# Performance work log

Hardware: AMD Instinct MI355X
Metric: run time of the kernel (lower is better)

The kernel has to match this reference:

```python
import jax, jax.numpy as jnp
import numpy as np

B, S, D, E, K = 4, 4096, 1024, 8, 2
H = 2 * D  # expert hidden dim


def setup_inputs() -> dict:
    key = jax.random.key(0)
    ks = jax.random.split(key, 7)
    scale = 0.02
    return {
        "x": jax.random.normal(ks[0], (B, S, D), dtype=jnp.float32),
        "router_w": jax.random.normal(ks[1], (D, E), dtype=jnp.float32) * scale,
        "router_b": jnp.zeros((E,), dtype=jnp.float32),
        "w1": jax.random.normal(ks[2], (E, D, H), dtype=jnp.float32) * scale,
        "b1": jnp.zeros((E, H), dtype=jnp.float32),
        "w2": jax.random.normal(ks[3], (E, H, D), dtype=jnp.float32) * scale,
        "b2": jnp.zeros((E, D), dtype=jnp.float32),
    }


def reference(x, router_w, router_b, w1, b1, w2, b2):
    # Router: softmax over experts, then top-k and renormalize
    logits = jnp.einsum("bsd,de->bse", x, router_w) + router_b
    probs = jax.nn.softmax(logits, axis=-1)
    top_p, top_i = jax.lax.top_k(probs, K)             # [B,S,K]
    top_p = top_p / jnp.sum(top_p, axis=-1, keepdims=True)

    out = jnp.zeros_like(x)
    for e in range(E):
        # gate weight for expert e per token (0 if not routed)
        gate = jnp.sum(top_p * (top_i == e), axis=-1)  # [B,S]
        h = jax.nn.relu(jnp.einsum("bsd,dh->bsh", x, w1[e]) + b1[e])
        y = jnp.einsum("bsh,hd->bsd", h, w2[e]) + b2[e]
        out = out + y * gate[..., None]
    return out
```

## Files before the change

kernel.cpp:

```cpp
#include <hip/hip_runtime.h>
#include <cstdio>
#include <cstdint>

#define N_TOK 16384
#define DIM   1024
#define NEXP  8
#define HID   2048
#define BK    32

typedef __attribute__((ext_vector_type(8))) short bf16x8;
typedef __attribute__((ext_vector_type(4))) float f32x4;

__device__ inline ushort f2bf(float f) {
  uint32_t u = __float_as_uint(f);
  uint32_t r = (u + 0x7fffu + ((u >> 16) & 1u)) >> 16;
  return (ushort)r;
}
__device__ inline float bf2f(ushort u) { return __uint_as_float(((uint32_t)u) << 16); }

__device__ __forceinline__ void gload_lds16(const void* g, void* l) {
  __builtin_amdgcn_global_load_lds((const __attribute__((address_space(1))) void*)g,
                                   (__attribute__((address_space(3))) void*)l, 16, 0, 0);
}

#define WAITV(N) asm volatile("s_waitcnt vmcnt(" #N ")" ::: "memory")
#define PBAR()  do { __builtin_amdgcn_s_barrier(); __builtin_amdgcn_sched_barrier(0); } while (0)

__global__ __launch_bounds__(256) void router_kernel(
    const float* __restrict__ x, const float* __restrict__ rw,
    const float* __restrict__ rb, int* __restrict__ blkcnt,
    int* __restrict__ tok_e, float* __restrict__ tok_g,
    ushort* __restrict__ xb) {
  __shared__ float wT[NEXP][DIM];
  __shared__ int hist[NEXP];
  if (threadIdx.x < NEXP) hist[threadIdx.x] = 0;
  for (int i = threadIdx.x; i < NEXP * DIM; i += 256) {
    int d = i >> 3, e = i & 7;
    wT[e][d] = rw[i];
  }
  __syncthreads();
  int wave = threadIdx.x >> 6, lane = threadIdx.x & 63;
  int t0 = blockIdx.x * 16 + wave * 4;
#pragma unroll
  for (int it = 0; it < 4; ++it) {
    int t = t0 + it;
    const float* xr = x + (size_t)t * DIM;
    float acc[NEXP];
#pragma unroll
    for (int e = 0; e < NEXP; ++e) acc[e] = 0.f;
#pragma unroll
    for (int j = 0; j < DIM / 64; ++j) {
      int d = lane + j * 64;
      float xv = xr[d];
#pragma unroll
      for (int e = 0; e < NEXP; ++e) acc[e] += xv * wT[e][d];
    }
    float lg[NEXP];
#pragma unroll
    for (int e = 0; e < NEXP; ++e) {
      float v = acc[e];
      for (int o = 32; o > 0; o >>= 1) v += __shfl_xor(v, o);
      lg[e] = v + rb[e];
    }
    int i0 = 0; float m0 = lg[0];
#pragma unroll
    for (int e = 1; e < NEXP; ++e) if (lg[e] > m0) { m0 = lg[e]; i0 = e; }
    int i1 = -1; float m1 = -3.4e38f;
#pragma unroll
    for (int e = 0; e < NEXP; ++e) if (e != i0 && lg[e] > m1) { m1 = lg[e]; i1 = e; }
    float g0 = 1.f / (1.f + expf(m1 - m0));
    float g1 = 1.f - g0;
    if (lane == 0) {
      tok_e[2 * t] = i0; tok_e[2 * t + 1] = i1;
      tok_g[2 * t] = g0; tok_g[2 * t + 1] = g1;
      atomicAdd(&hist[i0], 1); atomicAdd(&hist[i1], 1);
    }
  }
  {
    const float* xs = x + (size_t)blockIdx.x * 16 * DIM;
    ushort* xd = xb + (size_t)blockIdx.x * 16 * DIM;
    for (int i = threadIdx.x; i < 16 * DIM / 4; i += 256) {
      float4 v = *(const float4*)(xs + i * 4);
      ushort4 u = { f2bf(v.x), f2bf(v.y), f2bf(v.z), f2bf(v.w) };
      *(ushort4*)(xd + i * 4) = u;
    }
  }
  __syncthreads();
  if (threadIdx.x < NEXP) blkcnt[blockIdx.x * NEXP + threadIdx.x] = hist[threadIdx.x];
}

__global__ __launch_bounds__(512) void scan_kernel(const int* __restrict__ blkcnt,
                                                   int* __restrict__ blkbase,
                                                   int* __restrict__ offs) {
  __shared__ int s[64][8];
  __shared__ int chunkoff[64][8];
  __shared__ int offsh[8];
  int tid = threadIdx.x;
  int e = tid & 7, chunk = tid >> 3;
  int b0 = chunk * 16;
  int csum = 0;
#pragma unroll
  for (int b = 0; b < 16; ++b) csum += blkcnt[(b0 + b) * 8 + e];
  s[chunk][e] = csum;
  __syncthreads();
  int wave = tid >> 6, lane = tid & 63;
  int v = s[lane][wave];
  for (int o = 1; o < 64; o <<= 1) {
    int u = __shfl_up(v, o);
    if (lane >= o) v += u;
  }
  if (lane == 63) offsh[wave] = v;
  chunkoff[lane][wave] = v - s[lane][wave];
  __syncthreads();
  if (tid < 9) {
    int oe = 0;
    for (int j = 0; j < tid && j < 8; ++j) oe += offsh[j];
    offs[tid] = oe;
  }
  int oe2 = 0;
#pragma unroll
  for (int j = 0; j < 8; ++j) oe2 += (j < e) ? offsh[j] : 0;
  int base = oe2 + chunkoff[chunk][e];
  for (int b = 0; b < 16; ++b) {
    int idx = (b0 + b) * 8 + e;
    int c = blkcnt[idx];
    blkbase[idx] = base;
    base += c;
  }
}

__global__ __launch_bounds__(64) void gather_kernel(
    const int* __restrict__ tok_e, const float* __restrict__ tok_g,
    const int* __restrict__ blkbase, int* __restrict__ slot_token,
    float* __restrict__ slot_gate) {
  __shared__ int lcnt[NEXP];
  int tid = threadIdx.x, blk = blockIdx.x;
  if (tid < NEXP) lcnt[tid] = blkbase[blk * NEXP + tid];
  __syncthreads();
  if (tid < 32) {
    int t = blk * 16 + (tid >> 1);
    int k = tid & 1;
    int e = tok_e[2 * t + k];
    int s = atomicAdd(&lcnt[e], 1);
    slot_token[s] = t | (k << 16);
    slot_gate[s] = tok_g[2 * t + k];
  }
}

template <int R, int C>
__global__ __launch_bounds__(256) void transpose_cvt(const float* __restrict__ src,
                                                     ushort* __restrict__ dst) {
  __shared__ float tile[64][65];
  int e = blockIdx.z;
  const float* s = src + (size_t)e * R * C;
  ushort* d = dst + (size_t)e * R * C;
  int r0 = blockIdx.y * 64, c0 = blockIdx.x * 64;
  int tid = threadIdx.x;
#pragma unroll
  for (int i = 0; i < 4; ++i) {
    int idx = i * 256 + tid;
    int r = idx >> 4, c4 = (idx & 15) * 4;
    float4 v = *(const float4*)(s + (size_t)(r0 + r) * C + c0 + c4);
    tile[r][c4] = v.x; tile[r][c4 + 1] = v.y; tile[r][c4 + 2] = v.z; tile[r][c4 + 3] = v.w;
  }
  __syncthreads();
#pragma unroll
  for (int i = 0; i < 2; ++i) {
    int idx = i * 256 + tid;
    int orow = idx >> 3, g = (idx & 7) * 8;
    uint32_t p0 = (uint32_t)f2bf(tile[g + 0][orow]) | ((uint32_t)f2bf(tile[g + 1][orow]) << 16);
    uint32_t p1 = (uint32_t)f2bf(tile[g + 2][orow]) | ((uint32_t)f2bf(tile[g + 3][orow]) << 16);
    uint32_t p2 = (uint32_t)f2bf(tile[g + 4][orow]) | ((uint32_t)f2bf(tile[g + 5][orow]) << 16);
    uint32_t p3 = (uint32_t)f2bf(tile[g + 6][orow]) | ((uint32_t)f2bf(tile[g + 7][orow]) << 16);
    int4 v = { (int)p0, (int)p1, (int)p2, (int)p3 };
    *(int4*)(d + (size_t)(c0 + orow) * R + r0 + g) = v;
  }
}


__global__ __launch_bounds__(512, 1) void gemm1_kernel(
    const ushort* __restrict__ xb, const ushort* __restrict__ w1T,
    const float* __restrict__ b1, const int* __restrict__ offs,
    const int* __restrict__ slot_token, ushort* __restrict__ h) {
  int flat = blockIdx.x;
  int swz = (flat & 7) * 512 + (flat >> 3);
  int e = swz >> 9;
  int rem = swz & 511;
  int mt = rem >> 3;
  int nt = rem & 7;
  int off = offs[e];
  int cn = offs[e + 1] - off;
  if (mt * 256 >= cn) return;

  __shared__ __align__(16) ushort AB[4 * 16384];
  __shared__ int toks[256];
  int tid = threadIdx.x;
  if (tid < 256) {
    int r = mt * 256 + tid;
    toks[tid] = slot_token[off + (r < cn ? r : 0)] & 0xffff;
  }
  __syncthreads();
  int wave = tid >> 6, lane = tid & 63;
  int wm = (wave >> 2) * 128, wn = (wave & 3) * 64;

  const ushort* Bsrc = w1T + (size_t)e * HID * DIM + (size_t)(nt * 256) * DIM;
  int colsw = ((lane & 3) ^ ((lane >> 3) & 3)) * 8;
  int r0 = wave * 16 + (lane >> 2);
  const ushort* ag0 = xb + (size_t)toks[r0] * DIM + colsw;
  const ushort* ag1 = xb + (size_t)toks[128 + r0] * DIM + colsw;
  const ushort* bg0 = Bsrc + (size_t)r0 * DIM + colsw;
  const ushort* bg1 = Bsrc + (size_t)(128 + r0) * DIM + colsw;
  int ldsA0 = (wave * 16) * BK;
  int ldsA1 = (128 + wave * 16) * BK;
  int ldsB0 = 8192 + ldsA0;
  int ldsB1 = 8192 + ldsA1;

  f32x4 acc[8][4];
#pragma unroll
  for (int i = 0; i < 8; ++i)
#pragma unroll
    for (int j = 0; j < 4; ++j) acc[i][j] = (f32x4){0.f, 0.f, 0.f, 0.f};

  int rdo = (lane & 15) * 64 + ((((lane >> 4) & 3) << 4) ^ ((((lane & 15) >> 1) & 3) << 4));

  auto stage = [&](int buf) {
    ushort* lb = &AB[buf * 16384];
    gload_lds16(ag0, lb + ldsA0); ag0 += BK;
    gload_lds16(ag1, lb + ldsA1); ag1 += BK;
    gload_lds16(bg0, lb + ldsB0); bg0 += BK;
    gload_lds16(bg1, lb + ldsB1); bg1 += BK;
  };
  auto compute = [&](int buf) {
    const char* base = (const char*)AB + (size_t)buf * 32768;
    bf16x8 a[8], b[4];
#pragma unroll
    for (int mi = 0; mi < 8; ++mi)
      a[mi] = *(const bf16x8*)(base + (wm + mi * 16) * 64 + rdo);
#pragma unroll
    for (int ni = 0; ni < 4; ++ni)
      b[ni] = *(const bf16x8*)(base + 16384 + (wn + ni * 16) * 64 + rdo);
    __builtin_amdgcn_s_setprio(1);
#pragma unroll
    for (int mi = 0; mi < 8; ++mi)
#pragma unroll
      for (int ni = 0; ni < 4; ++ni)
        acc[mi][ni] = __builtin_amdgcn_mfma_f32_16x16x32_bf16(a[mi], b[ni], acc[mi][ni], 0, 0, 0);
    __builtin_amdgcn_s_setprio(0);
  };

  const int T = DIM / BK;
  stage(0); stage(1); stage(2);
  for (int t4 = 0; t4 < T - 4; t4 += 4) {
    WAITV(8); PBAR(); stage(3); compute(0);
    WAITV(8); PBAR(); stage(0); compute(1);
    WAITV(8); PBAR(); stage(1); compute(2);
    WAITV(8); PBAR(); stage(2); compute(3);
  }
  WAITV(8); PBAR(); stage(3); compute(0);
  WAITV(8); PBAR(); compute(1);
  WAITV(4); PBAR(); compute(2);
  WAITV(0); PBAR(); compute(3);

  __syncthreads();
  char* Cb = (char*)AB;
  int ln = lane & 15, lg4 = (lane >> 4) * 4;
#pragma unroll
  for (int ni = 0; ni < 4; ++ni) {
    int coll = wn + ni * 16 + ln;
    float bias = b1[(size_t)e * HID + nt * 256 + coll];
#pragma unroll
    for (int mi = 0; mi < 8; ++mi) {
#pragma unroll
      for (int rg = 0; rg < 4; ++rg) {
        int row = wm + mi * 16 + lg4 + rg;
        float v = fmaxf(acc[mi][ni][rg] + bias, 0.f);
        int slot = (coll >> 3) ^ (row & 7);
        *(ushort*)(Cb + row * 512 + slot * 16 + (coll & 7) * 2) = f2bf(v);
      }
    }
  }
  __syncthreads();
#pragma unroll
  for (int rr = 0; rr < 16; ++rr) {
    int row = rr * 16 + (tid >> 5);
    int scol = tid & 31;
    int4 v = *(const int4*)(Cb + row * 512 + ((scol ^ (row & 7)) << 4));
    int r = mt * 256 + row;
    if (r < cn)
      *(int4*)(h + (size_t)(off + r) * HID + nt * 256 + scol * 8) = v;
  }
}

__global__ __launch_bounds__(512, 1) void gemm2_kernel(
    const ushort* __restrict__ h, const ushort* __restrict__ w2T,
    const float* __restrict__ b2, const int* __restrict__ offs,
    const int* __restrict__ slot_token, const float* __restrict__ slot_gate,
    ushort* __restrict__ y) {
  int flat = blockIdx.x;
  int swz = (flat & 7) * 256 + (flat >> 3);
  int e = swz >> 8;
  int rem = swz & 255;
  int mt = rem >> 2;
  int nt = rem & 3;
  int off = offs[e];
  int cn = offs[e + 1] - off;
  if (mt * 256 >= cn) return;

  __shared__ __align__(16) ushort AB[4 * 16384];
  __shared__ int yrows[256];
  __shared__ float gts[256];
  int tid = threadIdx.x;
  if (tid < 256) {
    int r = mt * 256 + tid;
    int s = off + (r < cn ? r : 0);
    int tk = slot_token[s];
    yrows[tid] = ((tk & 0xffff) << 1) | (tk >> 16);
    gts[tid] = slot_gate[s];
  }
  __syncthreads();
  int wave = tid >> 6, lane = tid & 63;
  int wm = (wave >> 2) * 128, wn = (wave & 3) * 64;

  const ushort* Bsrc = w2T + (size_t)e * DIM * HID + (size_t)(nt * 256) * HID;
  int colsw = ((lane & 3) ^ ((lane >> 3) & 3)) * 8;
  int r0 = wave * 16 + (lane >> 2);
  int ra0 = mt * 256 + r0;       ra0 = ra0 < cn ? ra0 : 0;
  int ra1 = mt * 256 + 128 + r0; ra1 = ra1 < cn ? ra1 : 0;
  const ushort* ag0 = h + (size_t)(off + ra0) * HID + colsw;
  const ushort* ag1 = h + (size_t)(off + ra1) * HID + colsw;
  const ushort* bg0 = Bsrc + (size_t)r0 * HID + colsw;
  const ushort* bg1 = Bsrc + (size_t)(128 + r0) * HID + colsw;
  int ldsA0 = (wave * 16) * BK;
  int ldsA1 = (128 + wave * 16) * BK;
  int ldsB0 = 8192 + ldsA0;
  int ldsB1 = 8192 + ldsA1;

  f32x4 acc[8][4];
#pragma unroll
  for (int i = 0; i < 8; ++i)
#pragma unroll
    for (int j = 0; j < 4; ++j) acc[i][j] = (f32x4){0.f, 0.f, 0.f, 0.f};

  int rdo = (lane & 15) * 64 + ((((lane >> 4) & 3) << 4) ^ ((((lane & 15) >> 1) & 3) << 4));

  auto stage = [&](int buf) {
    ushort* lb = &AB[buf * 16384];
    gload_lds16(ag0, lb + ldsA0); ag0 += BK;
    gload_lds16(ag1, lb + ldsA1); ag1 += BK;
    gload_lds16(bg0, lb + ldsB0); bg0 += BK;
    gload_lds16(bg1, lb + ldsB1); bg1 += BK;
  };
  auto compute = [&](int buf) {
    const char* base = (const char*)AB + (size_t)buf * 32768;
    bf16x8 a[8], b[4];
#pragma unroll
    for (int mi = 0; mi < 8; ++mi)
      a[mi] = *(const bf16x8*)(base + (wm + mi * 16) * 64 + rdo);
#pragma unroll
    for (int ni = 0; ni < 4; ++ni)
      b[ni] = *(const bf16x8*)(base + 16384 + (wn + ni * 16) * 64 + rdo);
    __builtin_amdgcn_s_setprio(1);
#pragma unroll
    for (int mi = 0; mi < 8; ++mi)
#pragma unroll
      for (int ni = 0; ni < 4; ++ni)
        acc[mi][ni] = __builtin_amdgcn_mfma_f32_16x16x32_bf16(a[mi], b[ni], acc[mi][ni], 0, 0, 0);
    __builtin_amdgcn_s_setprio(0);
  };

  const int T = HID / BK;
  stage(0); stage(1); stage(2);
  for (int t4 = 0; t4 < T - 4; t4 += 4) {
    WAITV(8); PBAR(); stage(3); compute(0);
    WAITV(8); PBAR(); stage(0); compute(1);
    WAITV(8); PBAR(); stage(1); compute(2);
    WAITV(8); PBAR(); stage(2); compute(3);
  }
  WAITV(8); PBAR(); stage(3); compute(0);
  WAITV(8); PBAR(); compute(1);
  WAITV(4); PBAR(); compute(2);
  WAITV(0); PBAR(); compute(3);

  __syncthreads();
  char* Cb = (char*)AB;
  int ln = lane & 15, lg4 = (lane >> 4) * 4;
#pragma unroll
  for (int ni = 0; ni < 4; ++ni) {
    int coll = wn + ni * 16 + ln;
    float bias = b2[(size_t)e * DIM + nt * 256 + coll];
#pragma unroll
    for (int mi = 0; mi < 8; ++mi) {
#pragma unroll
      for (int rg = 0; rg < 4; ++rg) {
        int row = wm + mi * 16 + lg4 + rg;
        float v = gts[row] * (acc[mi][ni][rg] + bias);
        int slot = (coll >> 3) ^ (row & 7);
        *(ushort*)(Cb + row * 512 + slot * 16 + (coll & 7) * 2) = f2bf(v);
      }
    }
  }
  __syncthreads();
#pragma unroll
  for (int rr = 0; rr < 16; ++rr) {
    int row = rr * 16 + (tid >> 5);
    int scol = tid & 31;
    int4 v = *(const int4*)(Cb + row * 512 + ((scol ^ (row & 7)) << 4));
    int r = mt * 256 + row;
    if (r < cn)
      *(int4*)(y + (size_t)yrows[row] * DIM + nt * 256 + scol * 8) = v;
  }
}

__global__ __launch_bounds__(256) void combine_kernel(float* __restrict__ out) {
  int t = blockIdx.x;
  int d = threadIdx.x;
  const ushort* y = (const ushort*)out;
  ushort4 a = *(const ushort4*)(y + (size_t)(2 * t) * DIM + 4 * d);
  ushort4 b = *(const ushort4*)(y + (size_t)(2 * t + 1) * DIM + 4 * d);
  float4 r;
  r.x = bf2f(a.x) + bf2f(b.x);
  r.y = bf2f(a.y) + bf2f(b.y);
  r.z = bf2f(a.z) + bf2f(b.z);
  r.w = bf2f(a.w) + bf2f(b.w);
  __syncthreads();
  *(float4*)(out + (size_t)t * DIM + 4 * d) = r;
}

extern "C" void kernel_launch(void* const* d_in, const int* in_sizes, int n_in,
                              void* d_out, int out_size, void* d_ws, size_t ws_size,
                              hipStream_t stream) {
  const float* x  = (const float*)d_in[0];
  const float* rw = (const float*)d_in[1];
  const float* rb = (const float*)d_in[2];
  const float* w1 = (const float*)d_in[3];
  const float* b1 = (const float*)d_in[4];
  const float* w2 = (const float*)d_in[5];
  const float* b2 = (const float*)d_in[6];
  float* out = (float*)d_out;
  char* ws = (char*)d_ws;

  const size_t o_ctrl = 0;
  const size_t o_toke = 256;
  const size_t o_tokg = o_toke + 131072;
  const size_t o_stok = o_tokg + 131072;
  const size_t o_sgat = o_stok + 131072;
  const size_t o_xb   = o_sgat + 131072;
  const size_t o_w1T  = o_xb + (size_t)N_TOK * DIM * 2;
  const size_t o_h    = o_w1T + (size_t)NEXP * HID * DIM * 2;
  const size_t required = o_h + (size_t)N_TOK * 2 * HID * 2;
  if (ws_size < required) {
    fprintf(stderr, "kernel_launch: ws too small: have %zu need %zu\n", ws_size, required);
    return;
  }
  int* offs       = (int*)(ws + o_ctrl);
  int* tok_e      = (int*)(ws + o_toke);
  float* tok_g    = (float*)(ws + o_tokg);
  int* slot_token = (int*)(ws + o_stok);
  float* slot_gate= (float*)(ws + o_sgat);
  ushort* xb      = (ushort*)(ws + o_xb);
  ushort* w2T     = (ushort*)(ws + o_xb);
  ushort* w1T     = (ushort*)(ws + o_w1T);
  ushort* hbuf    = (ushort*)(ws + o_h);
  int* blkcnt     = (int*)(ws + o_h);
  int* blkbase    = blkcnt + 1024 * NEXP;


  router_kernel<<<N_TOK / 16, 256, 0, stream>>>(x, rw, rb, blkcnt, tok_e, tok_g, xb);
  scan_kernel<<<1, 512, 0, stream>>>(blkcnt, blkbase, offs);
  gather_kernel<<<N_TOK / 16, 64, 0, stream>>>(tok_e, tok_g, blkbase, slot_token, slot_gate);

  transpose_cvt<DIM, HID><<<dim3(HID / 64, DIM / 64, NEXP), 256, 0, stream>>>(w1, w1T);

  gemm1_kernel<<<8 * 64 * NEXP, 512, 0, stream>>>(xb, w1T, b1, offs, slot_token, hbuf);

  transpose_cvt<HID, DIM><<<dim3(DIM / 64, HID / 64, NEXP), 256, 0, stream>>>(w2, w2T);

  gemm2_kernel<<<4 * 64 * NEXP, 512, 0, stream>>>(hbuf, w2T, b2, offs, slot_token, slot_gate,
                                                  (ushort*)d_out);
  combine_kernel<<<N_TOK, 256, 0, stream>>>(out);
}
```

Before: 451.7 us.

## Interleave LDS fragment loads with MFMA in GEMMs; widen gather and combine blocks

Both GEMM compute steps now load A/B fragments from LDS in quarters, with MFMA groups issued between the loads. This lets LDS reads overlap matrix-core work and lowers peak fragment register pressure. Separately, the gather kernel packs four 64-thread groups per block, and the combine kernel handles two tokens per block with 16-byte bf16 loads. The LDS-interleave reorder may be undone by the compiler scheduler, so the main gain is uncertain.

```diff
diff --git a/kernel.cpp b/kernel.cpp
--- a/kernel.cpp
+++ b/kernel.cpp
@@ -129,19 +129,21 @@
   }
 }
 
-__global__ __launch_bounds__(64) void gather_kernel(
+__global__ __launch_bounds__(256) void gather_kernel(
     const int* __restrict__ tok_e, const float* __restrict__ tok_g,
     const int* __restrict__ blkbase, int* __restrict__ slot_token,
     float* __restrict__ slot_gate) {
-  __shared__ int lcnt[NEXP];
-  int tid = threadIdx.x, blk = blockIdx.x;
-  if (tid < NEXP) lcnt[tid] = blkbase[blk * NEXP + tid];
-  __syncthreads();
-  if (tid < 32) {
-    int t = blk * 16 + (tid >> 1);
-    int k = tid & 1;
+  __shared__ int lcnt[4][NEXP];
+  int grp = threadIdx.x >> 6;
+  int lane = threadIdx.x & 63;
+  int blk = blockIdx.x * 4 + grp;
+  if (lane < NEXP) lcnt[grp][lane] = blkbase[blk * NEXP + lane];
+  __syncthreads();
+  if (lane < 32) {
+    int t = blk * 16 + (lane >> 1);
+    int k = lane & 1;
     int e = tok_e[2 * t + k];
-    int s = atomicAdd(&lcnt[e], 1);
+    int s = atomicAdd(&lcnt[grp][e], 1);
     slot_token[s] = t | (k << 16);
     slot_gate[s] = tok_g[2 * t + k];
   }
@@ -232,18 +234,40 @@
   };
   auto compute = [&](int buf) {
     const char* base = (const char*)AB + (size_t)buf * 32768;
+    const char* bb = base + 16384;
     bf16x8 a[8], b[4];
 #pragma unroll
-    for (int mi = 0; mi < 8; ++mi)
-      a[mi] = *(const bf16x8*)(base + (wm + mi * 16) * 64 + rdo);
-#pragma unroll
-    for (int ni = 0; ni < 4; ++ni)
-      b[ni] = *(const bf16x8*)(base + 16384 + (wn + ni * 16) * 64 + rdo);
+    for (int mi = 0; mi < 4; ++mi) a[mi] = *(const bf16x8*)(base + (wm + mi * 16) * 64 + rdo);
+#pragma unroll
+    for (int ni = 0; ni < 2; ++ni) b[ni] = *(const bf16x8*)(bb + (wn + ni * 16) * 64 + rdo);
     __builtin_amdgcn_s_setprio(1);
 #pragma unroll
-    for (int mi = 0; mi < 8; ++mi)
-#pragma unroll
-      for (int ni = 0; ni < 4; ++ni)
+    for (int mi = 0; mi < 4; ++mi)
+#pragma unroll
+      for (int ni = 0; ni < 2; ++ni)
+        acc[mi][ni] = __builtin_amdgcn_mfma_f32_16x16x32_bf16(a[mi], b[ni], acc[mi][ni], 0, 0, 0);
+    __builtin_amdgcn_s_setprio(0);
+#pragma unroll
+    for (int ni = 2; ni < 4; ++ni) b[ni] = *(const bf16x8*)(bb + (wn + ni * 16) * 64 + rdo);
+    __builtin_amdgcn_s_setprio(1);
+#pragma unroll
+    for (int mi = 0; mi < 4; ++mi)
+#pragma unroll
+      for (int ni = 2; ni < 4; ++ni)
+        acc[mi][ni] = __builtin_amdgcn_mfma_f32_16x16x32_bf16(a[mi], b[ni], acc[mi][ni], 0, 0, 0);
+    __builtin_amdgcn_s_setprio(0);
+#pragma unroll
+    for (int mi = 4; mi < 8; ++mi) a[mi] = *(const bf16x8*)(base + (wm + mi * 16) * 64 + rdo);
+    __builtin_amdgcn_s_setprio(1);
+#pragma unroll
+    for (int mi = 4; mi < 8; ++mi)
+#pragma unroll
+      for (int ni = 2; ni < 4; ++ni)
+        acc[mi][ni] = __builtin_amdgcn_mfma_f32_16x16x32_bf16(a[mi], b[ni], acc[mi][ni], 0, 0, 0);
+#pragma unroll
+    for (int mi = 4; mi < 8; ++mi)
+#pragma unroll
+      for (int ni = 0; ni < 2; ++ni)
         acc[mi][ni] = __builtin_amdgcn_mfma_f32_16x16x32_bf16(a[mi], b[ni], acc[mi][ni], 0, 0, 0);
     __builtin_amdgcn_s_setprio(0);
   };
@@ -352,18 +376,40 @@
   };
   auto compute = [&](int buf) {
     const char* base = (const char*)AB + (size_t)buf * 32768;
+    const char* bb = base + 16384;
     bf16x8 a[8], b[4];
 #pragma unroll
-    for (int mi = 0; mi < 8; ++mi)
-      a[mi] = *(const bf16x8*)(base + (wm + mi * 16) * 64 + rdo);
-#pragma unroll
-    for (int ni = 0; ni < 4; ++ni)
-      b[ni] = *(const bf16x8*)(base + 16384 + (wn + ni * 16) * 64 + rdo);
+    for (int mi = 0; mi < 4; ++mi) a[mi] = *(const bf16x8*)(base + (wm + mi * 16) * 64 + rdo);
+#pragma unroll
+    for (int ni = 0; ni < 2; ++ni) b[ni] = *(const bf16x8*)(bb + (wn + ni * 16) * 64 + rdo);
     __builtin_amdgcn_s_setprio(1);
 #pragma unroll
-    for (int mi = 0; mi < 8; ++mi)
-#pragma unroll
-      for (int ni = 0; ni < 4; ++ni)
+    for (int mi = 0; mi < 4; ++mi)
+#pragma unroll
+      for (int ni = 0; ni < 2; ++ni)
+        acc[mi][ni] = __builtin_amdgcn_mfma_f32_16x16x32_bf16(a[mi], b[ni], acc[mi][ni], 0, 0, 0);
+    __builtin_amdgcn_s_setprio(0);
+#pragma unroll
+    for (int ni = 2; ni < 4; ++ni) b[ni] = *(const bf16x8*)(bb + (wn + ni * 16) * 64 + rdo);
+    __builtin_amdgcn_s_setprio(1);
+#pragma unroll
+    for (int mi = 0; mi < 4; ++mi)
+#pragma unroll
+      for (int ni = 2; ni < 4; ++ni)
+        acc[mi][ni] = __builtin_amdgcn_mfma_f32_16x16x32_bf16(a[mi], b[ni], acc[mi][ni], 0, 0, 0);
+    __builtin_amdgcn_s_setprio(0);
+#pragma unroll
+    for (int mi = 4; mi < 8; ++mi) a[mi] = *(const bf16x8*)(base + (wm + mi * 16) * 64 + rdo);
+    __builtin_amdgcn_s_setprio(1);
+#pragma unroll
+    for (int mi = 4; mi < 8; ++mi)
+#pragma unroll
+      for (int ni = 2; ni < 4; ++ni)
+        acc[mi][ni] = __builtin_amdgcn_mfma_f32_16x16x32_bf16(a[mi], b[ni], acc[mi][ni], 0, 0, 0);
+#pragma unroll
+    for (int mi = 4; mi < 8; ++mi)
+#pragma unroll
+      for (int ni = 0; ni < 2; ++ni)
         acc[mi][ni] = __builtin_amdgcn_mfma_f32_16x16x32_bf16(a[mi], b[ni], acc[mi][ni], 0, 0, 0);
     __builtin_amdgcn_s_setprio(0);
   };
@@ -412,18 +458,23 @@
 }
 
 __global__ __launch_bounds__(256) void combine_kernel(float* __restrict__ out) {
-  int t = blockIdx.x;
-  int d = threadIdx.x;
   const ushort* y = (const ushort*)out;
-  ushort4 a = *(const ushort4*)(y + (size_t)(2 * t) * DIM + 4 * d);
-  ushort4 b = *(const ushort4*)(y + (size_t)(2 * t + 1) * DIM + 4 * d);
-  float4 r;
-  r.x = bf2f(a.x) + bf2f(b.x);
-  r.y = bf2f(a.y) + bf2f(b.y);
-  r.z = bf2f(a.z) + bf2f(b.z);
-  r.w = bf2f(a.w) + bf2f(b.w);
-  __syncthreads();
-  *(float4*)(out + (size_t)t * DIM + 4 * d) = r;
+  int t = blockIdx.x * 2 + (threadIdx.x >> 7);
+  int c = (threadIdx.x & 127) * 8;
+  int4 av = *(const int4*)(y + (size_t)(2 * t) * DIM + c);
+  int4 bv = *(const int4*)(y + (size_t)(2 * t + 1) * DIM + c);
+  float4 r0, r1;
+  r0.x = bf2f((ushort)(av.x & 0xffff)) + bf2f((ushort)(bv.x & 0xffff));
+  r0.y = bf2f((ushort)((uint32_t)av.x >> 16)) + bf2f((ushort)((uint32_t)bv.x >> 16));
+  r0.z = bf2f((ushort)(av.y & 0xffff)) + bf2f((ushort)(bv.y & 0xffff));
+  r0.w = bf2f((ushort)((uint32_t)av.y >> 16)) + bf2f((ushort)((uint32_t)bv.y >> 16));
+  r1.x = bf2f((ushort)(av.z & 0xffff)) + bf2f((ushort)(bv.z & 0xffff));
+  r1.y = bf2f((ushort)((uint32_t)av.z >> 16)) + bf2f((ushort)((uint32_t)bv.z >> 16));
+  r1.z = bf2f((ushort)(av.w & 0xffff)) + bf2f((ushort)(bv.w & 0xffff));
+  r1.w = bf2f((ushort)((uint32_t)av.w >> 16)) + bf2f((ushort)((uint32_t)bv.w >> 16));
+  __syncthreads();
+  *(float4*)(out + (size_t)t * DIM + c) = r0;
+  *(float4*)(out + (size_t)t * DIM + c + 4) = r1;
 }
 
 extern "C" void kernel_launch(void* const* d_in, const int* in_sizes, int n_in,
@@ -467,7 +518,7 @@
 
   router_kernel<<<N_TOK / 16, 256, 0, stream>>>(x, rw, rb, blkcnt, tok_e, tok_g, xb);
   scan_kernel<<<1, 512, 0, stream>>>(blkcnt, blkbase, offs);
-  gather_kernel<<<N_TOK / 16, 64, 0, stream>>>(tok_e, tok_g, blkbase, slot_token, slot_gate);
+  gather_kernel<<<N_TOK / 64, 256, 0, stream>>>(tok_e, tok_g, blkbase, slot_token, slot_gate);
 
   transpose_cvt<DIM, HID><<<dim3(HID / 64, DIM / 64, NEXP), 256, 0, stream>>>(w1, w1T);
 
@@ -477,5 +528,5 @@
 
   gemm2_kernel<<<4 * 64 * NEXP, 512, 0, stream>>>(hbuf, w2T, b2, offs, slot_token, slot_gate,
                                                   (ushort*)d_out);
-  combine_kernel<<<N_TOK, 256, 0, stream>>>(out);
-}
+  combine_kernel<<<N_TOK / 2, 256, 0, stream>>>(out);
+}
```

Measured after the change: 453.6 us. About the same (+0.4%).
